# Performance work log

Hardware: AMD Instinct MI355X
Metric: run time of the kernel (lower is better)

Reference implementation:

```python
import jax, jax.numpy as jnp
import numpy as np

N_NODES = 100000
N_EDGES = 1600000
VOCAB = 1000
EMB_DIM = 64
OUT_DIM = 32


def setup_inputs() -> dict:
    key = jax.random.key(0)
    k1, k2, k3, k4, k5 = jax.random.split(key, 5)
    node_seq = jax.random.randint(k1, (N_NODES,), 0, VOCAB, dtype=jnp.int64)
    edge_index = jax.random.randint(k2, (2, N_EDGES), 0, N_NODES, dtype=jnp.int64)
    edge_weight = jax.random.uniform(k3, (N_EDGES,), dtype=jnp.float32)
    emb = jax.random.normal(k4, (VOCAB, EMB_DIM), dtype=jnp.float32)
    W = jax.random.normal(k5, (EMB_DIM, OUT_DIM), dtype=jnp.float32) * (1.0 / np.sqrt(EMB_DIM))
    b = jnp.zeros((OUT_DIM,), dtype=jnp.float32)
    return {"node_seq": node_seq, "edge_index": edge_index, "edge_weight": edge_weight,
            "emb": emb, "W": W, "b": b}


def reference(node_seq, edge_index, edge_weight, emb, W, b):
    N = node_seq.shape[0]
    # Embedding lookup: [N, EMB_DIM]
    x = emb[node_seq]
    # Linear transform first (GCNConv applies lin before propagate): [N, OUT_DIM]
    xw = x @ W
    # Add self loops with weight 1 (PyG GCNConv default add_self_loops=True, fill_value=1)
    loop = jnp.arange(N, dtype=edge_index.dtype)
    row = jnp.concatenate([edge_index[0], loop])
    col = jnp.concatenate([edge_index[1], loop])
    w = jnp.concatenate([edge_weight, jnp.ones((N,), dtype=edge_weight.dtype)])
    # Symmetric gcn_norm: deg over targets, norm = d^{-1/2}[row] * w * d^{-1/2}[col]
    deg = jax.ops.segment_sum(w, col, num_segments=N)
    dis = jnp.where(deg > 0, jax.lax.rsqrt(jnp.where(deg > 0, deg, 1.0)), 0.0)
    norm = dis[row] * w * dis[col]
    # Gather messages from source nodes, scale, scatter-add into targets
    msgs = norm[:, None] * xw[row]            # [E+N, OUT_DIM]
    out = jax.ops.segment_sum(msgs, col, num_segments=N) + b  # [N, OUT_DIM]
    # Mean pool over nodes
    return out.mean(axis=0)
```

## Files before the change

kernel.cpp:

```cpp
#include <hip/hip_runtime.h>

#define N_NODES 100000
#define N_EDGES 1600000
#define VOCAB   1000
#define EMB_DIM 64
#define OUT_DIM 32

#define BKT_BITS 9
#define BKT_SIZE 512
#define NBKT ((N_NODES + BKT_SIZE - 1) / BKT_SIZE)
#define CAP  12288
#define NSB  256
#define CHUNK (N_EDGES / NSB)

#define NBC 256
#define TBC 512

__device__ __forceinline__ void fatomic_add(float* p, float v) {
    unsafeAtomicAdd(p, v);
}


__global__ void k_init(int* __restrict__ cursors) {
    int i = blockIdx.x * blockDim.x + threadIdx.x;
    if (i < NBKT) cursors[i] = i * CAP;
}

__global__ void __launch_bounds__(256) k_scatter(
        const int* __restrict__ col, const float* __restrict__ w,
        int* __restrict__ cursors, uint2* __restrict__ recs) {
    __shared__ int lcnt[NBKT];
    __shared__ int lbase[NBKT];
    for (int i = threadIdx.x; i < NBKT; i += 256) lcnt[i] = 0;
    __syncthreads();
    const int e0 = blockIdx.x * CHUNK;
    for (int i = threadIdx.x; i < CHUNK; i += 256)
        atomicAdd(&lcnt[col[e0 + i] >> BKT_BITS], 1);
    __syncthreads();
    for (int i = threadIdx.x; i < NBKT; i += 256) {
        lbase[i] = atomicAdd(&cursors[i], lcnt[i]);
        lcnt[i] = 0;
    }
    __syncthreads();
    for (int i = threadIdx.x; i < CHUNK; i += 256) {
        int c = col[e0 + i];
        int b = c >> BKT_BITS;
        int pos = lbase[b] + atomicAdd(&lcnt[b], 1);
        recs[pos] = make_uint2((unsigned)c, __float_as_uint(w[e0 + i]));
    }
}

__global__ void __launch_bounds__(256) k_bucket_dis(
        const uint2* __restrict__ recs, const int* __restrict__ cursors,
        float* __restrict__ dis) {
    __shared__ float acc[BKT_SIZE];
    int b = blockIdx.x;
    for (int i = threadIdx.x; i < BKT_SIZE; i += 256) acc[i] = 0.0f;
    __syncthreads();
    const int base = b * CAP;
    const int cnt = cursors[b] - base;
    for (int i = threadIdx.x; i < cnt; i += 256) {
        uint2 r = recs[base + i];
        fatomic_add(&acc[(int)r.x - (b << BKT_BITS)], __uint_as_float(r.y));
    }
    __syncthreads();
    const int n0 = b << BKT_BITS;
    for (int i = threadIdx.x; i < BKT_SIZE && n0 + i < N_NODES; i += 256)
        dis[n0 + i] = __frsqrt_rn(1.0f + acc[i]);
}


__global__ void k_init_deg(float* __restrict__ deg) {
    int i = blockIdx.x * blockDim.x + threadIdx.x;
    if (i < N_NODES) deg[i] = 1.0f;
}
__global__ void k_deg(const int* __restrict__ col, const float* __restrict__ w,
                      float* __restrict__ deg) {
    int i = blockIdx.x * blockDim.x + threadIdx.x;
    if (i < N_EDGES) fatomic_add(&deg[col[i]], w[i]);
}
__global__ void k_dis(float* __restrict__ deg) {
    int i = blockIdx.x * blockDim.x + threadIdx.x;
    if (i < N_NODES) deg[i] = __frsqrt_rn(deg[i]);
}


__global__ void __launch_bounds__(TBC) k_coeff(
        const int* __restrict__ row, const int* __restrict__ col,
        const float* __restrict__ w, const float* __restrict__ dis,
        const int* __restrict__ node_seq, float* __restrict__ gcoeff) {
    __shared__ float lc[VOCAB];
    for (int i = threadIdx.x; i < VOCAB; i += TBC) lc[i] = 0.0f;
    __syncthreads();
    const int total = N_EDGES + N_NODES;
    const int stride = NBC * TBC;
    for (int i = blockIdx.x * TBC + threadIdx.x; i < total; i += stride) {
        if (i < N_EDGES) {
            int r = row[i];
            float norm = dis[r] * w[i] * dis[col[i]];
            fatomic_add(&lc[node_seq[r]], norm);
        } else {
            int n = i - N_EDGES;
            float d = dis[n];
            fatomic_add(&lc[node_seq[n]], d * d);
        }
    }
    __syncthreads();
    for (int i = threadIdx.x; i < VOCAB; i += TBC)
        gcoeff[blockIdx.x * VOCAB + i] = lc[i];
}

__global__ void __launch_bounds__(256) k_reduce(
        const float* __restrict__ gcoeff, float* __restrict__ coeff) {
    int g = blockIdx.x * 256 + threadIdx.x;
    int v = g >> 6;
    int l = g & 63;
    if (v >= VOCAB) return;
    float s = 0.0f;
    for (int b = l; b < NBC; b += 64) s += gcoeff[b * VOCAB + v];
    for (int off = 32; off > 0; off >>= 1) s += __shfl_down(s, off, 64);
    if (l == 0) coeff[v] = s;
}

__global__ void __launch_bounds__(1024) k_final(
        const float* __restrict__ coeff, const float* __restrict__ emb,
        const float* __restrict__ W, const float* __restrict__ bias,
        float* __restrict__ out) {
    __shared__ float lc[VOCAB];
    __shared__ float tk[16 * 64];
    int t = threadIdx.x;
    for (int v = t; v < VOCAB; v += 1024) lc[v] = coeff[v];
    __syncthreads();

    int k = t & 63;
    int g = t >> 6;
    float p = 0.0f;
    for (int v = g; v < VOCAB; v += 16) p += lc[v] * emb[v * EMB_DIM + k];
    tk[g * 64 + k] = p;
    __syncthreads();

    if (t < 64) {
        float s = 0.0f;
        for (int gg = 0; gg < 16; ++gg) s += tk[gg * 64 + t];
        tk[t] = s;
    }
    __syncthreads();

    if (t < OUT_DIM) {
        float s = 0.0f;
        for (int kk = 0; kk < EMB_DIM; ++kk) s += tk[kk] * W[kk * OUT_DIM + t];
        out[t] = s * (1.0f / (float)N_NODES) + bias[t];
    }
}

extern "C" void kernel_launch(void* const* d_in, const int* in_sizes, int n_in,
                              void* d_out, int out_size, void* d_ws, size_t ws_size,
                              hipStream_t stream) {
    const int*   node_seq = (const int*)  d_in[0];
    const int*   eidx     = (const int*)  d_in[1];
    const float* ew       = (const float*)d_in[2];
    const float* emb      = (const float*)d_in[3];
    const float* W        = (const float*)d_in[4];
    const float* b        = (const float*)d_in[5];
    float*       out      = (float*)d_out;

    const int* row = eidx;
    const int* col = eidx + N_EDGES;

    char* wsb = (char*)d_ws;
    const size_t REC_BYTES = (size_t)NBKT * CAP * sizeof(uint2);
    const size_t need = REC_BYTES + 1024 + (size_t)N_NODES * 4
                      + (size_t)NBC * VOCAB * 4 + 4096;

    if (ws_size >= need) {
        uint2* recs    = (uint2*)wsb;
        int*   cursors = (int*)(wsb + REC_BYTES);
        float* dis     = (float*)(wsb + REC_BYTES + 1024);
        float* gcoeff  = dis + N_NODES;
        float* coeff   = gcoeff + (size_t)NBC * VOCAB;

        k_init<<<1, 256, 0, stream>>>(cursors);
        k_scatter<<<NSB, 256, 0, stream>>>(col, ew, cursors, recs);
        k_bucket_dis<<<NBKT, 256, 0, stream>>>(recs, cursors, dis);
        k_coeff<<<NBC, TBC, 0, stream>>>(row, col, ew, dis, node_seq, gcoeff);
        k_reduce<<<(VOCAB * 64 + 255) / 256, 256, 0, stream>>>(gcoeff, coeff);
        k_final<<<1, 1024, 0, stream>>>(coeff, emb, W, b, out);
    } else {
        float* dis    = (float*)wsb;
        float* gcoeff = dis + N_NODES;
        float* coeff  = gcoeff + (size_t)NBC * VOCAB;

        k_init_deg<<<(N_NODES + 255) / 256, 256, 0, stream>>>(dis);
        k_deg<<<(N_EDGES + 255) / 256, 256, 0, stream>>>(col, ew, dis);
        k_dis<<<(N_NODES + 255) / 256, 256, 0, stream>>>(dis);
        k_coeff<<<NBC, TBC, 0, stream>>>(row, col, ew, dis, node_seq, gcoeff);
        k_reduce<<<(VOCAB * 64 + 255) / 256, 256, 0, stream>>>(gcoeff, coeff);
        k_final<<<1, 1024, 0, stream>>>(coeff, emb, W, b, out);
    }
}
```

Baseline: 156.7 us.

## Bucket edges by source row to compute per-node coefficients with shared-memory accumulation

The scatter kernel now bins every edge twice, by target bucket and by source bucket, packing local indices into the records. A new per-bucket coefficient kernel sums w*dis[col] per source node in shared memory, then folds each node's total into a per-bucket vocab histogram. This replaces the streaming coeff kernel, whose random shared atomics hit node_seq[row] on every edge. In exchange the scatter writes twice as much record data, the workspace doubles, the reduce step now sums NBKT partials, and the scatter block count goes up.

```diff
diff --git a/kernel.cpp b/kernel.cpp
--- a/kernel.cpp
+++ b/kernel.cpp
@@ -10,7 +10,7 @@
 #define BKT_SIZE 512
 #define NBKT ((N_NODES + BKT_SIZE - 1) / BKT_SIZE)
 #define CAP  12288
-#define NSB  256
+#define NSB  512
 #define CHUNK (N_EDGES / NSB)
 
 #define NBC 256
@@ -20,48 +20,55 @@
     unsafeAtomicAdd(p, v);
 }
 
-
 __global__ void k_init(int* __restrict__ cursors) {
     int i = blockIdx.x * blockDim.x + threadIdx.x;
-    if (i < NBKT) cursors[i] = i * CAP;
-}
-
-__global__ void __launch_bounds__(256) k_scatter(
-        const int* __restrict__ col, const float* __restrict__ w,
-        int* __restrict__ cursors, uint2* __restrict__ recs) {
-    __shared__ int lcnt[NBKT];
-    __shared__ int lbase[NBKT];
-    for (int i = threadIdx.x; i < NBKT; i += 256) lcnt[i] = 0;
+    if (i < 2 * NBKT) cursors[i] = (i < NBKT ? i : i - NBKT) * CAP;
+}
+
+__global__ void __launch_bounds__(256) k_scatter2(
+        const int* __restrict__ row, const int* __restrict__ col,
+        const float* __restrict__ w, int* __restrict__ cursors,
+        uint2* __restrict__ colrec, uint2* __restrict__ rowrec) {
+    __shared__ int cC[NBKT], cR[NBKT], bC[NBKT], bR[NBKT];
+    for (int i = threadIdx.x; i < NBKT; i += 256) { cC[i] = 0; cR[i] = 0; }
     __syncthreads();
     const int e0 = blockIdx.x * CHUNK;
-    for (int i = threadIdx.x; i < CHUNK; i += 256)
-        atomicAdd(&lcnt[col[e0 + i] >> BKT_BITS], 1);
+    for (int i = threadIdx.x; i < CHUNK; i += 256) {
+        atomicAdd(&cC[col[e0 + i] >> BKT_BITS], 1);
+        atomicAdd(&cR[row[e0 + i] >> BKT_BITS], 1);
+    }
     __syncthreads();
     for (int i = threadIdx.x; i < NBKT; i += 256) {
-        lbase[i] = atomicAdd(&cursors[i], lcnt[i]);
-        lcnt[i] = 0;
+        bC[i] = atomicAdd(&cursors[i], cC[i]);
+        bR[i] = atomicAdd(&cursors[NBKT + i], cR[i]);
+        cC[i] = 0; cR[i] = 0;
     }
     __syncthreads();
     for (int i = threadIdx.x; i < CHUNK; i += 256) {
         int c = col[e0 + i];
-        int b = c >> BKT_BITS;
-        int pos = lbase[b] + atomicAdd(&lcnt[b], 1);
-        recs[pos] = make_uint2((unsigned)c, __float_as_uint(w[e0 + i]));
+        int r = row[e0 + i];
+        unsigned ww = __float_as_uint(w[e0 + i]);
+        int pb = c >> BKT_BITS;
+        colrec[bC[pb] + atomicAdd(&cC[pb], 1)] =
+            make_uint2((unsigned)(c & (BKT_SIZE - 1)), ww);
+        int rb = r >> BKT_BITS;
+        rowrec[bR[rb] + atomicAdd(&cR[rb], 1)] =
+            make_uint2((unsigned)c | ((unsigned)(r & (BKT_SIZE - 1)) << 17), ww);
     }
 }
 
 __global__ void __launch_bounds__(256) k_bucket_dis(
-        const uint2* __restrict__ recs, const int* __restrict__ cursors,
+        const uint2* __restrict__ colrec, const int* __restrict__ cursors,
         float* __restrict__ dis) {
     __shared__ float acc[BKT_SIZE];
-    int b = blockIdx.x;
+    const int b = blockIdx.x;
     for (int i = threadIdx.x; i < BKT_SIZE; i += 256) acc[i] = 0.0f;
     __syncthreads();
     const int base = b * CAP;
     const int cnt = cursors[b] - base;
     for (int i = threadIdx.x; i < cnt; i += 256) {
-        uint2 r = recs[base + i];
-        fatomic_add(&acc[(int)r.x - (b << BKT_BITS)], __uint_as_float(r.y));
+        uint2 r = colrec[base + i];
+        fatomic_add(&acc[r.x], __uint_as_float(r.y));
     }
     __syncthreads();
     const int n0 = b << BKT_BITS;
@@ -69,6 +76,37 @@
         dis[n0 + i] = __frsqrt_rn(1.0f + acc[i]);
 }
 
+__global__ void __launch_bounds__(512) k_bucket_coeff(
+        const uint2* __restrict__ rowrec, const int* __restrict__ cursors,
+        const float* __restrict__ dis, const int* __restrict__ node_seq,
+        float* __restrict__ gcoeff) {
+    __shared__ float sacc[BKT_SIZE];
+    __shared__ float lc[VOCAB];
+    const int b = blockIdx.x;
+    for (int i = threadIdx.x; i < BKT_SIZE; i += 512) sacc[i] = 0.0f;
+    for (int i = threadIdx.x; i < VOCAB; i += 512) lc[i] = 0.0f;
+    __syncthreads();
+    const int base = b * CAP;
+    const int cnt = cursors[NBKT + b] - base;
+    for (int i = threadIdx.x; i < cnt; i += 512) {
+        uint2 rec = rowrec[base + i];
+        int c  = rec.x & 0x1FFFF;
+        int lr = rec.x >> 17;
+        fatomic_add(&sacc[lr], __uint_as_float(rec.y) * dis[c]);
+    }
+    __syncthreads();
+    const int n0 = b << BKT_BITS;
+    for (int i = threadIdx.x; i < BKT_SIZE; i += 512) {
+        int n = n0 + i;
+        if (n < N_NODES) {
+            float d = dis[n];
+            fatomic_add(&lc[node_seq[n]], d * (sacc[i] + d));
+        }
+    }
+    __syncthreads();
+    for (int i = threadIdx.x; i < VOCAB; i += 512)
+        gcoeff[b * VOCAB + i] = lc[i];
+}
 
 __global__ void k_init_deg(float* __restrict__ deg) {
     int i = blockIdx.x * blockDim.x + threadIdx.x;
@@ -83,9 +121,7 @@
     int i = blockIdx.x * blockDim.x + threadIdx.x;
     if (i < N_NODES) deg[i] = __frsqrt_rn(deg[i]);
 }
-
-
-__global__ void __launch_bounds__(TBC) k_coeff(
+__global__ void __launch_bounds__(TBC) k_coeff_stream(
         const int* __restrict__ row, const int* __restrict__ col,
         const float* __restrict__ w, const float* __restrict__ dis,
         const int* __restrict__ node_seq, float* __restrict__ gcoeff) {
@@ -97,8 +133,7 @@
     for (int i = blockIdx.x * TBC + threadIdx.x; i < total; i += stride) {
         if (i < N_EDGES) {
             int r = row[i];
-            float norm = dis[r] * w[i] * dis[col[i]];
-            fatomic_add(&lc[node_seq[r]], norm);
+            fatomic_add(&lc[node_seq[r]], dis[r] * w[i] * dis[col[i]]);
         } else {
             int n = i - N_EDGES;
             float d = dis[n];
@@ -111,13 +146,13 @@
 }
 
 __global__ void __launch_bounds__(256) k_reduce(
-        const float* __restrict__ gcoeff, float* __restrict__ coeff) {
+        const float* __restrict__ gcoeff, float* __restrict__ coeff, int npart) {
     int g = blockIdx.x * 256 + threadIdx.x;
     int v = g >> 6;
     int l = g & 63;
     if (v >= VOCAB) return;
     float s = 0.0f;
-    for (int b = l; b < NBC; b += 64) s += gcoeff[b * VOCAB + v];
+    for (int p = l; p < npart; p += 64) s += gcoeff[p * VOCAB + v];
     for (int off = 32; off > 0; off >>= 1) s += __shfl_down(s, off, 64);
     if (l == 0) coeff[v] = s;
 }
@@ -169,21 +204,22 @@
 
     char* wsb = (char*)d_ws;
     const size_t REC_BYTES = (size_t)NBKT * CAP * sizeof(uint2);
-    const size_t need = REC_BYTES + 1024 + (size_t)N_NODES * 4
-                      + (size_t)NBC * VOCAB * 4 + 4096;
+    const size_t need = 2 * REC_BYTES + 4096 + (size_t)N_NODES * 4
+                      + (size_t)NBKT * VOCAB * 4 + VOCAB * 4 + 4096;
 
     if (ws_size >= need) {
-        uint2* recs    = (uint2*)wsb;
-        int*   cursors = (int*)(wsb + REC_BYTES);
-        float* dis     = (float*)(wsb + REC_BYTES + 1024);
+        uint2* colrec  = (uint2*)wsb;
+        uint2* rowrec  = (uint2*)(wsb + REC_BYTES);
+        int*   cursors = (int*)(wsb + 2 * REC_BYTES);
+        float* dis     = (float*)(wsb + 2 * REC_BYTES + 4096);
         float* gcoeff  = dis + N_NODES;
-        float* coeff   = gcoeff + (size_t)NBC * VOCAB;
-
-        k_init<<<1, 256, 0, stream>>>(cursors);
-        k_scatter<<<NSB, 256, 0, stream>>>(col, ew, cursors, recs);
-        k_bucket_dis<<<NBKT, 256, 0, stream>>>(recs, cursors, dis);
-        k_coeff<<<NBC, TBC, 0, stream>>>(row, col, ew, dis, node_seq, gcoeff);
-        k_reduce<<<(VOCAB * 64 + 255) / 256, 256, 0, stream>>>(gcoeff, coeff);
+        float* coeff   = gcoeff + (size_t)NBKT * VOCAB;
+
+        k_init<<<2, 256, 0, stream>>>(cursors);
+        k_scatter2<<<NSB, 256, 0, stream>>>(row, col, ew, cursors, colrec, rowrec);
+        k_bucket_dis<<<NBKT, 256, 0, stream>>>(colrec, cursors, dis);
+        k_bucket_coeff<<<NBKT, 512, 0, stream>>>(rowrec, cursors, dis, node_seq, gcoeff);
+        k_reduce<<<(VOCAB * 64 + 255) / 256, 256, 0, stream>>>(gcoeff, coeff, NBKT);
         k_final<<<1, 1024, 0, stream>>>(coeff, emb, W, b, out);
     } else {
         float* dis    = (float*)wsb;
@@ -193,8 +229,8 @@
         k_init_deg<<<(N_NODES + 255) / 256, 256, 0, stream>>>(dis);
         k_deg<<<(N_EDGES + 255) / 256, 256, 0, stream>>>(col, ew, dis);
         k_dis<<<(N_NODES + 255) / 256, 256, 0, stream>>>(dis);
-        k_coeff<<<NBC, TBC, 0, stream>>>(row, col, ew, dis, node_seq, gcoeff);
-        k_reduce<<<(VOCAB * 64 + 255) / 256, 256, 0, stream>>>(gcoeff, coeff);
+        k_coeff_stream<<<NBC, TBC, 0, stream>>>(row, col, ew, dis, node_seq, gcoeff);
+        k_reduce<<<(VOCAB * 64 + 255) / 256, 256, 0, stream>>>(gcoeff, coeff, NBC);
         k_final<<<1, 1024, 0, stream>>>(coeff, emb, W, b, out);
     }
 }
```

New measurement: 163.7 us. 1.04x slower.
